# Kernel optimization log

Measured on AMD Instinct MI355X. Metric: run time of the kernel, lower is better.

## Reference

```python
import jax, jax.numpy as jnp
import numpy as np

B, T, HID = 1, 4096, 1024
H, HKV, D = 16, 4, 64          # query heads, kv heads, head_dim
G = H // HKV                    # gqa groups; repeat '(h g)' -> q head idx = h*G + g
EPS = 1e-6
SCALE = 1.0 / np.sqrt(D)


def setup_inputs() -> dict:
    key = jax.random.key(0)
    ks = jax.random.split(key, 8)
    hidden_states = jax.random.normal(ks[0], (B, T, HID), dtype=jnp.float32)
    # real rotary tables, shape [1, T, D//2]
    inv_freq = 1.0 / (10000.0 ** (jnp.arange(0, D // 2, dtype=jnp.float32) / (D // 2)))
    theta = jnp.arange(T, dtype=jnp.float32)[:, None] * inv_freq[None, :]
    cos = jnp.cos(theta)[None]
    sin = jnp.sin(theta)[None]
    s = 1.0 / np.sqrt(HID)
    Wq = jax.random.normal(ks[1], (HID, H * D), dtype=jnp.float32) * s
    Wk = jax.random.normal(ks[2], (HID, HKV * D), dtype=jnp.float32) * s
    Wv = jax.random.normal(ks[3], (HID, HKV * D), dtype=jnp.float32) * s
    Wo = jax.random.normal(ks[4], (H * D, HID), dtype=jnp.float32) * s
    q_norm_w = jnp.ones((D,), dtype=jnp.float32)
    k_norm_w = jnp.ones((D,), dtype=jnp.float32)
    return dict(hidden_states=hidden_states, cos=cos, sin=sin, Wq=Wq, Wk=Wk,
                Wv=Wv, Wo=Wo, q_norm_w=q_norm_w, k_norm_w=k_norm_w)


def _rmsnorm(x, w):
    xf = x.astype(jnp.float32)
    n = xf * jax.lax.rsqrt(jnp.mean(xf * xf, axis=-1, keepdims=True) + EPS)
    return (n * w).astype(x.dtype)


def _rope(x, cos, sin):
    # x: [b, t, h, d]; cos/sin: [1, t, d//2] -> [1, t, 1, d//2]
    half = x.shape[-1] // 2
    x1, x2 = x[..., :half], x[..., half:]
    c = cos[:, :x.shape[1], None, :]
    s = sin[:, :x.shape[1], None, :]
    return jnp.concatenate([x1 * c - x2 * s, x1 * s + x2 * c], axis=-1)


def reference(hidden_states, cos, sin, Wq, Wk, Wv, Wo, q_norm_w, k_norm_w):
    b, t, _ = hidden_states.shape
    q = (hidden_states @ Wq).reshape(b, t, H, D)
    k = (hidden_states @ Wk).reshape(b, t, HKV, D)
    v = (hidden_states @ Wv).reshape(b, t, HKV, D)
    q = _rmsnorm(q, q_norm_w)
    k = _rmsnorm(k, k_norm_w)
    q = _rope(q, cos, sin)
    k = _rope(k, cos, sin)
    # GQA without materializing repeated K/V: q head idx = kv_head*G + group
    qg = q.reshape(b, t, HKV, G, D)
    scores = jnp.einsum('bqhgd,bkhd->bhgqk', qg, k) * SCALE
    causal = jnp.tril(jnp.ones((t, t), dtype=bool))  # flex block_mask = causal decoder mask
    scores = jnp.where(causal, scores, jnp.finfo(scores.dtype).min)
    p = jax.nn.softmax(scores, axis=-1)
    out = jnp.einsum('bhgqk,bkhd->bqhgd', p, v).reshape(b, t, H * D)
    return out @ Wo
```

## Files before the change

kernel.cpp:

```cpp
#include <hip/hip_runtime.h>
#include <stdint.h>

#define TT 4096
#define HIDD 1024

typedef __attribute__((ext_vector_type(4))) float f32x4;
typedef __attribute__((ext_vector_type(8))) short s16x8;

static constexpr float kEps = 1e-6f;
static constexpr float kCsc = 0.125f * 1.44269504088896f;

static constexpr size_t OFF_HS   = 0;
static constexpr size_t OFF_WQKV = 8388608;
static constexpr size_t OFF_WO   = 11534336;
static constexpr size_t OFF_QKV  = 13631488;
static constexpr size_t OFF_Q    = 0;
static constexpr size_t OFF_K    = 8388608;
static constexpr size_t OFF_VT   = 38797312;
static constexpr size_t OFF_O    = 13631488;

__device__ __forceinline__ unsigned int pk_bf16(float a, float b) {
  union { float f; unsigned int u; } x, y;
  x.f = a; y.f = b;
  unsigned int lo = (x.u + 0x7fffu + ((x.u >> 16) & 1u)) >> 16;
  unsigned int hi = (y.u + 0x7fffu + ((y.u >> 16) & 1u)) >> 16;
  return (lo & 0xffffu) | (hi << 16);
}
__device__ __forceinline__ unsigned short bf16_1(float a) {
  union { float f; unsigned int u; } x; x.f = a;
  return (unsigned short)((x.u + 0x7fffu + ((x.u >> 16) & 1u)) >> 16);
}
__device__ __forceinline__ unsigned int cvtpk(float lo, float hi) {
  unsigned int r;
  asm("v_cvt_pk_bf16_f32 %0, %1, %2" : "=v"(r) : "v"(lo), "v"(hi));
  return r;
}
__device__ __forceinline__ void gload16(const void* g, void* l) {
  __builtin_amdgcn_global_load_lds(
      (const __attribute__((address_space(1))) unsigned int*)g,
      (__attribute__((address_space(3))) unsigned int*)l, 16, 0, 0);
}

__global__ void k_convert_hs(const float* __restrict__ hs, unsigned short* __restrict__ out) {
  int idx = blockIdx.x * 256 + threadIdx.x;
  int t = idx >> 7, kc = idx & 127;
  const float4* src = (const float4*)(hs + (size_t)t * HIDD + kc * 8);
  float4 a = src[0], b = src[1];
  int kcs = (kc & ~7) | ((kc & 7) ^ (t & 7));
  uint4 w;
  w.x = pk_bf16(a.x, a.y); w.y = pk_bf16(a.z, a.w);
  w.z = pk_bf16(b.x, b.y); w.w = pk_bf16(b.z, b.w);
  *(uint4*)(out + (size_t)t * HIDD + kcs * 8) = w;
}

__global__ void k_convert_w_all(const float* __restrict__ Wq, const float* __restrict__ Wk,
                                const float* __restrict__ Wv, const float* __restrict__ Wo,
                                unsigned short* __restrict__ wqkv, unsigned short* __restrict__ wo_t) {
  int b = blockIdx.x, tid = threadIdx.x;
  const float* W; unsigned short* outT; int nshift, idx;
  if (b < 512)      { W = Wq; outT = wqkv;                nshift = 10; idx = b * 256 + tid; }
  else if (b < 640) { W = Wk; outT = wqkv + 1024 * 1024;  nshift = 8;  idx = (b - 512) * 256 + tid; }
  else if (b < 768) { W = Wv; outT = wqkv + 1280 * 1024;  nshift = 8;  idx = (b - 640) * 256 + tid; }
  else              { W = Wo; outT = wo_t;                nshift = 10; idx = (b - 768) * 256 + tid; }
  int ncols = 1 << nshift;
  int kc = idx >> nshift, n = idx & (ncols - 1);
  float v[8];
#pragma unroll
  for (int e = 0; e < 8; ++e) v[e] = W[(size_t)(kc * 8 + e) * ncols + n];
  int kcs = (kc & ~7) | ((kc & 7) ^ (n & 7));
  uint4 w;
  w.x = pk_bf16(v[0], v[1]); w.y = pk_bf16(v[2], v[3]);
  w.z = pk_bf16(v[4], v[5]); w.w = pk_bf16(v[6], v[7]);
  *(uint4*)(outT + (size_t)n * HIDD + kcs * 8) = w;
}

__global__ __launch_bounds__(256) void k_gemm(const unsigned short* __restrict__ A,
                                              const unsigned short* __restrict__ Bt,
                                              float* __restrict__ C, int M, int N, int K) {
  __shared__ __attribute__((aligned(16))) unsigned short As[2][128 * 64];
  __shared__ __attribute__((aligned(16))) unsigned short Bs[2][64 * 64];
  const int tid = threadIdx.x;
  const int m0 = blockIdx.y * 128, n0 = blockIdx.x * 64;
  const int wid = tid >> 6, lane = tid & 63;
  const int g = lane >> 4, qi = lane & 15;
  const int wr = wid >> 1, wc = wid & 1;
  const int srow = lane >> 3, schk = lane & 7;
  f32x4 acc[4][2] = {};
  const int nkt = K >> 6;

  auto STAGE = [&](int b, int k0) {
#pragma unroll
    for (int j = 0; j < 4; ++j) {
      int ra = j * 32 + wid * 8 + srow;
      gload16(A + (size_t)(m0 + ra) * K + k0 + schk * 8,
              (char*)&As[b][0] + j * 4096 + (wid << 10));
    }
#pragma unroll
    for (int j = 0; j < 2; ++j) {
      int rb = j * 32 + wid * 8 + srow;
      gload16(Bt + (size_t)(n0 + rb) * K + k0 + schk * 8,
              (char*)&Bs[b][0] + j * 4096 + (wid << 10));
    }
  };

  STAGE(0, 0);
  __syncthreads();
  int cur = 0;
  for (int kt = 0; kt < nkt; ++kt) {
    if (kt + 1 < nkt) STAGE(cur ^ 1, (kt + 1) << 6);
#pragma unroll
    for (int kh = 0; kh < 2; ++kh) {
      s16x8 af[4], bq[2];
#pragma unroll
      for (int i = 0; i < 4; ++i) {
        int rA = wr * 64 + i * 16 + qi;
        af[i] = *(const s16x8*)((const char*)&As[cur][0] + rA * 128 + ((((kh << 2) | g) ^ (rA & 7)) << 4));
      }
#pragma unroll
      for (int jn = 0; jn < 2; ++jn) {
        int rB = wc * 32 + jn * 16 + qi;
        bq[jn] = *(const s16x8*)((const char*)&Bs[cur][0] + rB * 128 + ((((kh << 2) | g) ^ (rB & 7)) << 4));
      }
      __builtin_amdgcn_s_setprio(1);
#pragma unroll
      for (int i = 0; i < 4; ++i)
#pragma unroll
        for (int jn = 0; jn < 2; ++jn)
          acc[i][jn] = __builtin_amdgcn_mfma_f32_16x16x32_bf16(af[i], bq[jn], acc[i][jn], 0, 0, 0);
      __builtin_amdgcn_s_setprio(0);
    }
    __syncthreads();
    cur ^= 1;
  }
#pragma unroll
  for (int i = 0; i < 4; ++i)
#pragma unroll
    for (int jn = 0; jn < 2; ++jn) {
      int row = m0 + wr * 64 + i * 16 + g * 4;
      int col = n0 + wc * 32 + jn * 16 + qi;
#pragma unroll
      for (int r = 0; r < 4; ++r)
        C[(size_t)(row + r) * N + col] = acc[i][jn][r];
    }
}

__global__ void k_prep(const float* __restrict__ qkv, const float* __restrict__ cosb,
                       const float* __restrict__ sinb, const float* __restrict__ qw,
                       const float* __restrict__ kw, unsigned short* __restrict__ qo,
                       unsigned short* __restrict__ ko) {
  int rowid = blockIdx.x * 4 + (threadIdx.x >> 6);
  int lane = threadIdx.x & 63;
  int t = rowid / 20, slot = rowid % 20;
  float x = qkv[(size_t)t * 1536 + slot * 64 + lane];
  float ss = x * x;
#pragma unroll
  for (int off = 32; off; off >>= 1) ss += __shfl_xor(ss, off);
  float n = x * rsqrtf(ss * (1.0f / 64.0f) + kEps);
  n *= (slot < 16) ? qw[lane] : kw[lane];
  float c = cosb[t * 32 + (lane & 31)];
  float s = sinb[t * 32 + (lane & 31)];
  float other = __shfl_xor(n, 32);
  float r = (lane < 32) ? (n * c - other * s) : (other * s + n * c);
  if (slot < 16) {
    unsigned short b = bf16_1(r * kCsc);
    qo[((size_t)slot * TT + t) * 64 + lane] = b;
  } else {
    unsigned short b = bf16_1(r);
    int hv = slot - 16;
    int d = (((lane >> 3) ^ (t & 7)) << 3) | (lane & 7);
    ko[((size_t)hv * TT + t) * 64 + d] = b;
  }
}

__global__ void k_vT(const float* __restrict__ qkv, unsigned short* __restrict__ vt) {
  __shared__ float tile[64][65];
  int t0 = blockIdx.x * 64, hv = blockIdx.y, tid = threadIdx.x;
  int cc = tid & 63, rr0 = tid >> 6;
#pragma unroll
  for (int i = 0; i < 16; ++i) {
    int r = rr0 * 16 + i;
    tile[r][cc] = qkv[(size_t)(t0 + r) * 1536 + 1280 + hv * 64 + cc];
  }
  __syncthreads();
#pragma unroll
  for (int jj = 0; jj < 2; ++jj) {
    int idx = jj * 256 + tid;
    int d = idx >> 3, tc = idx & 7;
    uint4 w;
    w.x = pk_bf16(tile[tc * 8 + 0][d], tile[tc * 8 + 1][d]);
    w.y = pk_bf16(tile[tc * 8 + 2][d], tile[tc * 8 + 3][d]);
    w.z = pk_bf16(tile[tc * 8 + 4][d], tile[tc * 8 + 5][d]);
    w.w = pk_bf16(tile[tc * 8 + 6][d], tile[tc * 8 + 7][d]);
    int tcs = tc ^ (d & 7);
    *(uint4*)(vt + ((size_t)hv * 64 + d) * TT + t0 + tcs * 8) = w;
  }
}

__global__ __launch_bounds__(512) void k_attn(const unsigned short* __restrict__ q,
                                              const unsigned short* __restrict__ kk,
                                              const unsigned short* __restrict__ vt,
                                              unsigned short* __restrict__ o) {
  __shared__ __attribute__((aligned(16))) unsigned short Kl[2][64 * 64];
  __shared__ __attribute__((aligned(16))) unsigned short Vl[2][64 * 64];
  __shared__ __attribute__((aligned(16))) unsigned short Pl[8][1536];
  const int tid = threadIdx.x;
  const int bid = blockIdx.x;
  const int work = (bid & 7) * 64 + (bid >> 3);
  const int h = work >> 5;
  const int i0 = work & 31;
  const int hv = h >> 2;
  const int wid = tid >> 6, lane = tid & 63, g = lane >> 4, qi = lane & 15;
  const int qt = (wid < 4) ? i0 : (63 - i0);
  const int smax = 63 - i0;
  char* pb = (char*)&Pl[wid][0];

  auto STAGE = [&](int b, int s) {
    const int kv0 = s * 64;
    const int r = wid * 8 + (lane >> 3), c8 = (lane & 7) * 8;
    gload16(kk + ((size_t)hv * TT + kv0 + r) * 64 + c8, (char*)&Kl[b][0] + (wid << 10));
    gload16(vt + ((size_t)hv * 64 + r) * TT + kv0 + c8, (char*)&Vl[b][0] + (wid << 10));
  };

  const int qg = qt * 64 + (wid & 3) * 16 + qi;
  s16x8 qf[2];
#pragma unroll
  for (int kh = 0; kh < 2; ++kh)
    qf[kh] = *(const s16x8*)(q + ((size_t)h * TT + qg) * 64 + kh * 32 + g * 8);
  f32x4 acc[4] = {};
  float l0 = 0.0f, l1 = 0.0f;

  STAGE(0, 0);
  __syncthreads();
  int cur = 0;
  for (int s = 0; s <= smax; ++s) {
    if (s < smax) STAGE(cur ^ 1, s + 1);
    if (s <= qt) {
      const int kv0 = s * 64;
      f32x4 sacc[4] = {};
#pragma unroll
      for (int kh = 0; kh < 2; ++kh) {
        s16x8 kf[4];
#pragma unroll
        for (int cf = 0; cf < 4; ++cf) {
          int row = cf * 16 + qi;
          kf[cf] = *(const s16x8*)((const char*)&Kl[cur][0] + row * 128 + ((((kh << 2) | g) ^ (row & 7)) << 4));
        }
        __builtin_amdgcn_s_setprio(1);
#pragma unroll
        for (int cf = 0; cf < 4; ++cf)
          sacc[cf] = __builtin_amdgcn_mfma_f32_16x16x32_bf16(kf[cf], qf[kh], sacc[cf], 0, 0, 0);
        __builtin_amdgcn_s_setprio(0);
      }
      float pv[16];
      if (s == qt) {
#pragma unroll
        for (int cf = 0; cf < 4; ++cf)
#pragma unroll
          for (int r = 0; r < 4; ++r) {
            float v = sacc[cf][r];
            if ((kv0 + cf * 16 + g * 4 + r) > qg) v = -1e30f;
            pv[cf * 4 + r] = v;
          }
      } else {
#pragma unroll
        for (int cf = 0; cf < 4; ++cf)
#pragma unroll
          for (int r = 0; r < 4; ++r) pv[cf * 4 + r] = sacc[cf][r];
      }
#pragma unroll
      for (int i = 0; i < 8; ++i) {
        float e0 = exp2f(pv[2 * i]), e1 = exp2f(pv[2 * i + 1]);
        pv[2 * i] = e0; pv[2 * i + 1] = e1;
        l0 += e0; l1 += e1;
      }
#pragma unroll
      for (int cf = 0; cf < 4; ++cf) {
        int chunk = cf * 2 + (g >> 1);
        int base = qi * 128 + ((chunk ^ (qi & 7)) << 4) + ((g & 1) << 3);
        uint2 pw;
        pw.x = cvtpk(pv[cf * 4 + 0], pv[cf * 4 + 1]);
        pw.y = cvtpk(pv[cf * 4 + 2], pv[cf * 4 + 3]);
        *(uint2*)(pb + base) = pw;
      }
#pragma unroll
      for (int kh = 0; kh < 2; ++kh) {
        s16x8 pf = *(const s16x8*)(pb + qi * 128 + ((((kh << 2) | g) ^ (qi & 7)) << 4));
        s16x8 vf[4];
#pragma unroll
        for (int cf = 0; cf < 4; ++cf) {
          int row = cf * 16 + qi;
          vf[cf] = *(const s16x8*)((const char*)&Vl[cur][0] + row * 128 + ((((kh << 2) | g) ^ (row & 7)) << 4));
        }
        __builtin_amdgcn_s_setprio(1);
#pragma unroll
        for (int cf = 0; cf < 4; ++cf)
          acc[cf] = __builtin_amdgcn_mfma_f32_16x16x32_bf16(vf[cf], pf, acc[cf], 0, 0, 0);
        __builtin_amdgcn_s_setprio(0);
      }
    }
    __syncthreads();
    cur ^= 1;
  }
  float l_run = l0 + l1;
  l_run += __shfl_xor(l_run, 16);
  l_run += __shfl_xor(l_run, 32);
  float inv = 1.0f / l_run;
#pragma unroll
  for (int cf = 0; cf < 4; ++cf) {
    int col = h * 64 + cf * 16 + g * 4;
    int chunk = col >> 3;
    int chs = (chunk & ~7) | ((chunk & 7) ^ (qg & 7));
    char* ob = (char*)o + (size_t)qg * 2048 + (chs << 4) + ((g & 1) << 3);
    *(unsigned int*)ob = cvtpk(acc[cf][0] * inv, acc[cf][1] * inv);
    *(unsigned int*)(ob + 4) = cvtpk(acc[cf][2] * inv, acc[cf][3] * inv);
  }
}

extern "C" void kernel_launch(void* const* d_in, const int* in_sizes, int n_in,
                              void* d_out, int out_size, void* d_ws, size_t ws_size,
                              hipStream_t stream) {
  const float* hs   = (const float*)d_in[0];
  const float* cosb = (const float*)d_in[1];
  const float* sinb = (const float*)d_in[2];
  const float* Wq   = (const float*)d_in[3];
  const float* Wk   = (const float*)d_in[4];
  const float* Wv   = (const float*)d_in[5];
  const float* Wo   = (const float*)d_in[6];
  const float* qw   = (const float*)d_in[7];
  const float* kw   = (const float*)d_in[8];
  char* ws = (char*)d_ws;
  unsigned short* hs_swz = (unsigned short*)(ws + OFF_HS);
  unsigned short* wqkv   = (unsigned short*)(ws + OFF_WQKV);
  unsigned short* wo_t   = (unsigned short*)(ws + OFF_WO);
  float*          qkv    = (float*)(ws + OFF_QKV);
  unsigned short* qbf    = (unsigned short*)(ws + OFF_Q);
  unsigned short* kbf    = (unsigned short*)(ws + OFF_K);
  unsigned short* vtb    = (unsigned short*)(ws + OFF_VT);
  unsigned short* obf    = (unsigned short*)(ws + OFF_O);

  k_convert_hs<<<2048, 256, 0, stream>>>(hs, hs_swz);
  k_convert_w_all<<<1280, 256, 0, stream>>>(Wq, Wk, Wv, Wo, wqkv, wo_t);
  k_gemm<<<dim3(24, 32), 256, 0, stream>>>(hs_swz, wqkv, qkv, 4096, 1536, 1024);
  k_prep<<<20480, 256, 0, stream>>>(qkv, cosb, sinb, qw, kw, qbf, kbf);
  k_vT<<<dim3(64, 4), 256, 0, stream>>>(qkv, vtb);
  k_attn<<<512, 512, 0, stream>>>(qbf, kbf, vtb, obf);
  k_gemm<<<dim3(16, 32), 256, 0, stream>>>(obf, wo_t, (float*)d_out, 4096, 1024, 1024);
}
```

Baseline: 141.0 us.

## Rewrite attention with 32x32x16 MFMA, register-resident P, and new work mapping

```diff
diff --git a/kernel.cpp b/kernel.cpp
--- a/kernel.cpp
+++ b/kernel.cpp
@@ -5,6 +5,7 @@
 #define HIDD 1024
 
 typedef __attribute__((ext_vector_type(4))) float f32x4;
+typedef __attribute__((ext_vector_type(16))) float f32x16;
 typedef __attribute__((ext_vector_type(8))) short s16x8;
 
 static constexpr float kEps = 1e-6f;
@@ -196,123 +197,124 @@
   }
 }
 
-__global__ __launch_bounds__(512) void k_attn(const unsigned short* __restrict__ q,
-                                              const unsigned short* __restrict__ kk,
-                                              const unsigned short* __restrict__ vt,
-                                              unsigned short* __restrict__ o) {
-  __shared__ __attribute__((aligned(16))) unsigned short Kl[2][64 * 64];
-  __shared__ __attribute__((aligned(16))) unsigned short Vl[2][64 * 64];
-  __shared__ __attribute__((aligned(16))) unsigned short Pl[8][1536];
+__global__ __launch_bounds__(256, 2) void k_attn(const unsigned short* __restrict__ q,
+                                                 const unsigned short* __restrict__ kk,
+                                                 const unsigned short* __restrict__ vt,
+                                                 unsigned short* __restrict__ o) {
+  __shared__ __attribute__((aligned(16))) char smem[57344];
   const int tid = threadIdx.x;
+  const int wid = tid >> 6, lane = tid & 63;
+  const int ln31 = lane & 31, hi = lane >> 5;
   const int bid = blockIdx.x;
-  const int work = (bid & 7) * 64 + (bid >> 3);
-  const int h = work >> 5;
-  const int i0 = work & 31;
-  const int hv = h >> 2;
-  const int wid = tid >> 6, lane = tid & 63, g = lane >> 4, qi = lane & 15;
-  const int qt = (wid < 4) ? i0 : (63 - i0);
-  const int smax = 63 - i0;
-  char* pb = (char*)&Pl[wid][0];
-
-  auto STAGE = [&](int b, int s) {
-    const int kv0 = s * 64;
-    const int r = wid * 8 + (lane >> 3), c8 = (lane & 7) * 8;
-    gload16(kk + ((size_t)hv * TT + kv0 + r) * 64 + c8, (char*)&Kl[b][0] + (wid << 10));
-    gload16(vt + ((size_t)hv * 64 + r) * TT + kv0 + c8, (char*)&Vl[b][0] + (wid << 10));
+  const int xcd = bid & 7;
+  const int s = bid >> 3;
+  const int hsel = s >> 5;
+  const int t0_ = (s & 31) ^ hsel;
+  const int j = (t0_ & 1) ? (t0_ >> 1) : (31 - (t0_ >> 1));
+  const int head = xcd * 2 + hsel;
+  const int hv = head >> 2;
+  const int u = 4 * j + wid;
+  const int qbase = u * 32;
+  const int eu = (u >> 1) + 1;
+  const int E = 2 * j + 2;
+
+  auto STAGE = [&](int b, int st) {
+    const int kv0 = st * 64;
+#pragma unroll
+    for (int p = 0; p < 2; ++p) {
+      int c = tid + p * 256;
+      int row = c >> 3, ch = c & 7;
+      gload16(kk + ((size_t)hv * TT + kv0 + row) * 64 + ch * 8,
+              smem + b * 8192 + c * 16);
+      gload16(vt + ((size_t)hv * 64 + row) * TT + kv0 + ch * 8,
+              smem + 16384 + b * 8192 + c * 16);
+    }
   };
 
-  const int qg = qt * 64 + (wid & 3) * 16 + qi;
-  s16x8 qf[2];
-#pragma unroll
-  for (int kh = 0; kh < 2; ++kh)
-    qf[kh] = *(const s16x8*)(q + ((size_t)h * TT + qg) * 64 + kh * 32 + g * 8);
-  f32x4 acc[4] = {};
-  float l0 = 0.0f, l1 = 0.0f;
+  s16x8 qf[4];
+#pragma unroll
+  for (int ks = 0; ks < 4; ++ks)
+    qf[ks] = *(const s16x8*)(q + ((size_t)head * TT + qbase + ln31) * 64 + ks * 16 + hi * 8);
+
+  f32x16 oacc[2] = {};
+  float lp0 = 0.0f, lp1 = 0.0f;
 
   STAGE(0, 0);
   __syncthreads();
   int cur = 0;
-  for (int s = 0; s <= smax; ++s) {
-    if (s < smax) STAGE(cur ^ 1, s + 1);
-    if (s <= qt) {
-      const int kv0 = s * 64;
-      f32x4 sacc[4] = {};
-#pragma unroll
-      for (int kh = 0; kh < 2; ++kh) {
-        s16x8 kf[4];
-#pragma unroll
-        for (int cf = 0; cf < 4; ++cf) {
-          int row = cf * 16 + qi;
-          kf[cf] = *(const s16x8*)((const char*)&Kl[cur][0] + row * 128 + ((((kh << 2) | g) ^ (row & 7)) << 4));
+  for (int st = 0; st < E; ++st) {
+    if (st + 1 < E) STAGE(cur ^ 1, st + 1);
+    if (st < eu) {
+      const int kv0 = st * 64;
+      const char* Kb = smem + cur * 8192;
+      const char* Vb = smem + 16384 + cur * 8192;
+      f32x16 sacc[2] = {};
+#pragma unroll
+      for (int T = 0; T < 2; ++T) {
+#pragma unroll
+        for (int ks = 0; ks < 4; ++ks) {
+          int row = T * 32 + ln31;
+          s16x8 kf = *(const s16x8*)(Kb + row * 128 + (((2 * ks + hi) ^ (row & 7)) << 4));
+          sacc[T] = __builtin_amdgcn_mfma_f32_32x32x16_bf16(kf, qf[ks], sacc[T], 0, 0, 0);
         }
-        __builtin_amdgcn_s_setprio(1);
-#pragma unroll
-        for (int cf = 0; cf < 4; ++cf)
-          sacc[cf] = __builtin_amdgcn_mfma_f32_16x16x32_bf16(kf[cf], qf[kh], sacc[cf], 0, 0, 0);
-        __builtin_amdgcn_s_setprio(0);
-      }
-      float pv[16];
-      if (s == qt) {
-#pragma unroll
-        for (int cf = 0; cf < 4; ++cf)
-#pragma unroll
-          for (int r = 0; r < 4; ++r) {
-            float v = sacc[cf][r];
-            if ((kv0 + cf * 16 + g * 4 + r) > qg) v = -1e30f;
-            pv[cf * 4 + r] = v;
+      }
+      float pv[32];
+      const bool diag = (st == eu - 1);
+      const int qg = qbase + ln31;
+#pragma unroll
+      for (int T = 0; T < 2; ++T)
+#pragma unroll
+        for (int r = 0; r < 16; ++r) {
+          float v = sacc[T][r];
+          if (diag) {
+            int kvg = kv0 + T * 32 + (r & 3) + 8 * (r >> 2) + 4 * hi;
+            if (kvg > qg) v = -1e30f;
           }
-      } else {
-#pragma unroll
-        for (int cf = 0; cf < 4; ++cf)
-#pragma unroll
-          for (int r = 0; r < 4; ++r) pv[cf * 4 + r] = sacc[cf][r];
-      }
-#pragma unroll
-      for (int i = 0; i < 8; ++i) {
-        float e0 = exp2f(pv[2 * i]), e1 = exp2f(pv[2 * i + 1]);
-        pv[2 * i] = e0; pv[2 * i + 1] = e1;
-        l0 += e0; l1 += e1;
-      }
-#pragma unroll
-      for (int cf = 0; cf < 4; ++cf) {
-        int chunk = cf * 2 + (g >> 1);
-        int base = qi * 128 + ((chunk ^ (qi & 7)) << 4) + ((g & 1) << 3);
-        uint2 pw;
-        pw.x = cvtpk(pv[cf * 4 + 0], pv[cf * 4 + 1]);
-        pw.y = cvtpk(pv[cf * 4 + 2], pv[cf * 4 + 3]);
-        *(uint2*)(pb + base) = pw;
-      }
-#pragma unroll
-      for (int kh = 0; kh < 2; ++kh) {
-        s16x8 pf = *(const s16x8*)(pb + qi * 128 + ((((kh << 2) | g) ^ (qi & 7)) << 4));
-        s16x8 vf[4];
-#pragma unroll
-        for (int cf = 0; cf < 4; ++cf) {
-          int row = cf * 16 + qi;
-          vf[cf] = *(const s16x8*)((const char*)&Vl[cur][0] + row * 128 + ((((kh << 2) | g) ^ (row & 7)) << 4));
+          float e = exp2f(v);
+          pv[T * 16 + r] = e;
+          if (r & 1) lp1 += e; else lp0 += e;
         }
-        __builtin_amdgcn_s_setprio(1);
-#pragma unroll
-        for (int cf = 0; cf < 4; ++cf)
-          acc[cf] = __builtin_amdgcn_mfma_f32_16x16x32_bf16(vf[cf], pf, acc[cf], 0, 0, 0);
-        __builtin_amdgcn_s_setprio(0);
+      s16x8 pa[4];
+#pragma unroll
+      for (int ks = 0; ks < 4; ++ks) {
+        const float* pg = pv + ks * 8;
+        unsigned w0 = cvtpk(pg[0], pg[1]);
+        unsigned w1 = cvtpk(pg[2], pg[3]);
+        unsigned w2 = cvtpk(pg[4], pg[5]);
+        unsigned w3 = cvtpk(pg[6], pg[7]);
+        asm("v_permlane32_swap_b32 %0, %1" : "+v"(w0), "+v"(w2));
+        asm("v_permlane32_swap_b32 %0, %1" : "+v"(w1), "+v"(w3));
+        union { uint4 u4; s16x8 v8; } cc;
+        cc.u4.x = w0; cc.u4.y = w1; cc.u4.z = w2; cc.u4.w = w3;
+        pa[ks] = cc.v8;
+      }
+#pragma unroll
+      for (int D = 0; D < 2; ++D) {
+#pragma unroll
+        for (int ks = 0; ks < 4; ++ks) {
+          int row = D * 32 + ln31;
+          s16x8 vf = *(const s16x8*)(Vb + row * 128 + (((2 * ks + hi) ^ (row & 7)) << 4));
+          oacc[D] = __builtin_amdgcn_mfma_f32_32x32x16_bf16(pa[ks], vf, oacc[D], 0, 0, 0);
+        }
       }
     }
     __syncthreads();
     cur ^= 1;
   }
-  float l_run = l0 + l1;
-  l_run += __shfl_xor(l_run, 16);
-  l_run += __shfl_xor(l_run, 32);
-  float inv = 1.0f / l_run;
-#pragma unroll
-  for (int cf = 0; cf < 4; ++cf) {
-    int col = h * 64 + cf * 16 + g * 4;
-    int chunk = col >> 3;
-    int chs = (chunk & ~7) | ((chunk & 7) ^ (qg & 7));
-    char* ob = (char*)o + (size_t)qg * 2048 + (chs << 4) + ((g & 1) << 3);
-    *(unsigned int*)ob = cvtpk(acc[cf][0] * inv, acc[cf][1] * inv);
-    *(unsigned int*)(ob + 4) = cvtpk(acc[cf][2] * inv, acc[cf][3] * inv);
+  float lfull = lp0 + lp1;
+  lfull += __shfl_xor(lfull, 32);
+  float invl = 1.0f / lfull;
+#pragma unroll
+  for (int r = 0; r < 16; ++r) {
+    int qoff = (r & 3) + 8 * (r >> 2) + 4 * hi;
+    float il = __shfl(invl, qoff);
+    int q_g = qbase + qoff;
+    size_t rowb = (size_t)q_g * 2048 + head * 128 + (lane & 7) * 2;
+#pragma unroll
+    for (int D = 0; D < 2; ++D) {
+      int ch = ((4 * D + (ln31 >> 3)) ^ (q_g & 7)) << 4;
+      *(unsigned short*)((char*)o + rowb + ch) = bf16_1(oacc[D][r] * il);
+    }
   }
 }
 
@@ -343,6 +345,6 @@
   k_gemm<<<dim3(24, 32), 256, 0, stream>>>(hs_swz, wqkv, qkv, 4096, 1536, 1024);
   k_prep<<<20480, 256, 0, stream>>>(qkv, cosb, sinb, qw, kw, qbf, kbf);
   k_vT<<<dim3(64, 4), 256, 0, stream>>>(qkv, vtb);
-  k_attn<<<512, 512, 0, stream>>>(qbf, kbf, vtb, obf);
+  k_attn<<<512, 256, 0, stream>>>(qbf, kbf, vtb, obf);
   k_gemm<<<dim3(16, 32), 256, 0, stream>>>(obf, wo_t, (float*)d_out, 4096, 1024, 1024);
 }
```

Result: slower. 169.8 us (+20.5%).

## Fuse QK RMSnorm+RoPE and V transpose into QKV GEMM epilogue

Applied to the files above, without the earlier changes.

```diff
diff --git a/kernel.cpp b/kernel.cpp
--- a/kernel.cpp
+++ b/kernel.cpp
@@ -13,11 +13,10 @@
 static constexpr size_t OFF_HS   = 0;
 static constexpr size_t OFF_WQKV = 8388608;
 static constexpr size_t OFF_WO   = 11534336;
-static constexpr size_t OFF_QKV  = 13631488;
-static constexpr size_t OFF_Q    = 0;
-static constexpr size_t OFF_K    = 8388608;
+static constexpr size_t OFF_Q    = 13631488;
+static constexpr size_t OFF_K    = 22020096;
+static constexpr size_t OFF_O    = 24117248;
 static constexpr size_t OFF_VT   = 38797312;
-static constexpr size_t OFF_O    = 13631488;
 
 __device__ __forceinline__ unsigned int pk_bf16(float a, float b) {
   union { float f; unsigned int u; } x, y;
@@ -25,10 +24,6 @@
   unsigned int lo = (x.u + 0x7fffu + ((x.u >> 16) & 1u)) >> 16;
   unsigned int hi = (y.u + 0x7fffu + ((y.u >> 16) & 1u)) >> 16;
   return (lo & 0xffffu) | (hi << 16);
-}
-__device__ __forceinline__ unsigned short bf16_1(float a) {
-  union { float f; unsigned int u; } x; x.f = a;
-  return (unsigned short)((x.u + 0x7fffu + ((x.u >> 16) & 1u)) >> 16);
 }
 __device__ __forceinline__ unsigned int cvtpk(float lo, float hi) {
   unsigned int r;
@@ -72,6 +67,148 @@
   w.x = pk_bf16(v[0], v[1]); w.y = pk_bf16(v[2], v[3]);
   w.z = pk_bf16(v[4], v[5]); w.w = pk_bf16(v[6], v[7]);
   *(uint4*)(outT + (size_t)n * HIDD + kcs * 8) = w;
+}
+
+__global__ __launch_bounds__(256) void k_gemm_qkv(const unsigned short* __restrict__ A,
+                                                  const unsigned short* __restrict__ Bt,
+                                                  const float* __restrict__ cosb,
+                                                  const float* __restrict__ sinb,
+                                                  const float* __restrict__ qw,
+                                                  const float* __restrict__ kw,
+                                                  unsigned short* __restrict__ qo,
+                                                  unsigned short* __restrict__ ko,
+                                                  unsigned short* __restrict__ vt) {
+  __shared__ __attribute__((aligned(16))) char smem[49152];
+  const int K = HIDD;
+  const int tid = threadIdx.x;
+  const int m0 = blockIdx.y * 128, slot = blockIdx.x, n0 = slot * 64;
+  const int wid = tid >> 6, lane = tid & 63;
+  const int g = lane >> 4, qi = lane & 15;
+  const int wr = wid >> 1, wc = wid & 1;
+  const int srow = lane >> 3, schk = lane & 7;
+  f32x4 acc[4][2] = {};
+  const int nkt = K >> 6;
+
+  auto STAGE = [&](int b, int k0) {
+#pragma unroll
+    for (int j = 0; j < 4; ++j) {
+      int ra = j * 32 + wid * 8 + srow;
+      gload16(A + (size_t)(m0 + ra) * K + k0 + schk * 8,
+              smem + b * 16384 + j * 4096 + (wid << 10));
+    }
+#pragma unroll
+    for (int j = 0; j < 2; ++j) {
+      int rb = j * 32 + wid * 8 + srow;
+      gload16(Bt + (size_t)(n0 + rb) * K + k0 + schk * 8,
+              smem + 32768 + b * 8192 + j * 4096 + (wid << 10));
+    }
+  };
+
+  STAGE(0, 0);
+  __syncthreads();
+  int cur = 0;
+  for (int kt = 0; kt < nkt; ++kt) {
+    if (kt + 1 < nkt) STAGE(cur ^ 1, (kt + 1) << 6);
+#pragma unroll
+    for (int kh = 0; kh < 2; ++kh) {
+      s16x8 af[4], bq[2];
+#pragma unroll
+      for (int i = 0; i < 4; ++i) {
+        int rA = wr * 64 + i * 16 + qi;
+        af[i] = *(const s16x8*)(smem + cur * 16384 + rA * 128 + ((((kh << 2) | g) ^ (rA & 7)) << 4));
+      }
+#pragma unroll
+      for (int jn = 0; jn < 2; ++jn) {
+        int rB = wc * 32 + jn * 16 + qi;
+        bq[jn] = *(const s16x8*)(smem + 32768 + cur * 8192 + rB * 128 + ((((kh << 2) | g) ^ (rB & 7)) << 4));
+      }
+      __builtin_amdgcn_s_setprio(1);
+#pragma unroll
+      for (int i = 0; i < 4; ++i)
+#pragma unroll
+        for (int jn = 0; jn < 2; ++jn)
+          acc[i][jn] = __builtin_amdgcn_mfma_f32_16x16x32_bf16(af[i], bq[jn], acc[i][jn], 0, 0, 0);
+      __builtin_amdgcn_s_setprio(0);
+    }
+    __syncthreads();
+    cur ^= 1;
+  }
+
+  float* Cs = (float*)smem;
+#pragma unroll
+  for (int i = 0; i < 4; ++i)
+#pragma unroll
+    for (int jn = 0; jn < 2; ++jn) {
+      int row = wr * 64 + i * 16 + g * 4;
+      int col = wc * 32 + jn * 16 + qi;
+#pragma unroll
+      for (int r = 0; r < 4; ++r)
+        Cs[(row + r) * 66 + col] = acc[i][jn][r];
+    }
+  __syncthreads();
+
+  if (slot < 20) {
+    const int lr = tid >> 1, hf = tid & 1;
+    const int t = m0 + lr;
+    const float* self_p = Cs + lr * 66 + hf * 32;
+    const float* oth_p  = Cs + lr * 66 + (1 - hf) * 32;
+    float ss = 0.0f;
+#pragma unroll
+    for (int e = 0; e < 32; ++e) { float v = self_p[e]; ss += v * v; }
+    ss += __shfl_xor(ss, 1);
+    const float rms = rsqrtf(ss * (1.0f / 64.0f) + kEps);
+    const float* wvec = (slot < 16) ? qw : kw;
+    const float outscale = (slot < 16) ? kCsc : 1.0f;
+    unsigned int u[16];
+#pragma unroll
+    for (int ee = 0; ee < 16; ++ee) {
+      float o2[2];
+#pragma unroll
+      for (int p = 0; p < 2; ++p) {
+        int e = 2 * ee + p;
+        float c = cosb[t * 32 + e];
+        float s = sinb[t * 32 + e];
+        float self = self_p[e] * rms * wvec[hf * 32 + e];
+        float oth  = oth_p[e]  * rms * wvec[(1 - hf) * 32 + e];
+        float r = hf ? (oth * s + self * c) : (self * c - oth * s);
+        o2[p] = r * outscale;
+      }
+      u[ee] = cvtpk(o2[0], o2[1]);
+    }
+    if (slot < 16) {
+      unsigned short* base = qo + ((size_t)slot * TT + t) * 64 + hf * 32;
+#pragma unroll
+      for (int cidx = 0; cidx < 4; ++cidx) {
+        uint4 w; w.x = u[cidx * 4]; w.y = u[cidx * 4 + 1]; w.z = u[cidx * 4 + 2]; w.w = u[cidx * 4 + 3];
+        *(uint4*)(base + cidx * 8) = w;
+      }
+    } else {
+      const int hv = slot - 16;
+      unsigned short* base = ko + ((size_t)hv * TT + t) * 64;
+#pragma unroll
+      for (int cidx = 0; cidx < 4; ++cidx) {
+        int gc = hf * 4 + cidx;
+        uint4 w; w.x = u[cidx * 4]; w.y = u[cidx * 4 + 1]; w.z = u[cidx * 4 + 2]; w.w = u[cidx * 4 + 3];
+        *(uint4*)(base + (gc ^ (t & 7)) * 8) = w;
+      }
+    }
+  } else {
+    const int hv = slot - 20;
+#pragma unroll
+    for (int tt = 0; tt < 2; ++tt)
+#pragma unroll
+      for (int jj = 0; jj < 2; ++jj) {
+        int idx = jj * 256 + tid;
+        int d = idx >> 3, tc = idx & 7;
+        uint4 w;
+        w.x = cvtpk(Cs[(tt * 64 + tc * 8 + 0) * 66 + d], Cs[(tt * 64 + tc * 8 + 1) * 66 + d]);
+        w.y = cvtpk(Cs[(tt * 64 + tc * 8 + 2) * 66 + d], Cs[(tt * 64 + tc * 8 + 3) * 66 + d]);
+        w.z = cvtpk(Cs[(tt * 64 + tc * 8 + 4) * 66 + d], Cs[(tt * 64 + tc * 8 + 5) * 66 + d]);
+        w.w = cvtpk(Cs[(tt * 64 + tc * 8 + 6) * 66 + d], Cs[(tt * 64 + tc * 8 + 7) * 66 + d]);
+        int tcs = tc ^ (d & 7);
+        *(uint4*)(vt + ((size_t)hv * 64 + d) * TT + m0 + tt * 64 + tcs * 8) = w;
+      }
+  }
 }
 
 __global__ __launch_bounds__(256) void k_gemm(const unsigned short* __restrict__ A,
@@ -142,58 +279,6 @@
       for (int r = 0; r < 4; ++r)
         C[(size_t)(row + r) * N + col] = acc[i][jn][r];
     }
-}
-
-__global__ void k_prep(const float* __restrict__ qkv, const float* __restrict__ cosb,
-                       const float* __restrict__ sinb, const float* __restrict__ qw,
-                       const float* __restrict__ kw, unsigned short* __restrict__ qo,
-                       unsigned short* __restrict__ ko) {
-  int rowid = blockIdx.x * 4 + (threadIdx.x >> 6);
-  int lane = threadIdx.x & 63;
-  int t = rowid / 20, slot = rowid % 20;
-  float x = qkv[(size_t)t * 1536 + slot * 64 + lane];
-  float ss = x * x;
-#pragma unroll
-  for (int off = 32; off; off >>= 1) ss += __shfl_xor(ss, off);
-  float n = x * rsqrtf(ss * (1.0f / 64.0f) + kEps);
-  n *= (slot < 16) ? qw[lane] : kw[lane];
-  float c = cosb[t * 32 + (lane & 31)];
-  float s = sinb[t * 32 + (lane & 31)];
-  float other = __shfl_xor(n, 32);
-  float r = (lane < 32) ? (n * c - other * s) : (other * s + n * c);
-  if (slot < 16) {
-    unsigned short b = bf16_1(r * kCsc);
-    qo[((size_t)slot * TT + t) * 64 + lane] = b;
-  } else {
-    unsigned short b = bf16_1(r);
-    int hv = slot - 16;
-    int d = (((lane >> 3) ^ (t & 7)) << 3) | (lane & 7);
-    ko[((size_t)hv * TT + t) * 64 + d] = b;
-  }
-}
-
-__global__ void k_vT(const float* __restrict__ qkv, unsigned short* __restrict__ vt) {
-  __shared__ float tile[64][65];
-  int t0 = blockIdx.x * 64, hv = blockIdx.y, tid = threadIdx.x;
-  int cc = tid & 63, rr0 = tid >> 6;
-#pragma unroll
-  for (int i = 0; i < 16; ++i) {
-    int r = rr0 * 16 + i;
-    tile[r][cc] = qkv[(size_t)(t0 + r) * 1536 + 1280 + hv * 64 + cc];
-  }
-  __syncthreads();
-#pragma unroll
-  for (int jj = 0; jj < 2; ++jj) {
-    int idx = jj * 256 + tid;
-    int d = idx >> 3, tc = idx & 7;
-    uint4 w;
-    w.x = pk_bf16(tile[tc * 8 + 0][d], tile[tc * 8 + 1][d]);
-    w.y = pk_bf16(tile[tc * 8 + 2][d], tile[tc * 8 + 3][d]);
-    w.z = pk_bf16(tile[tc * 8 + 4][d], tile[tc * 8 + 5][d]);
-    w.w = pk_bf16(tile[tc * 8 + 6][d], tile[tc * 8 + 7][d]);
-    int tcs = tc ^ (d & 7);
-    *(uint4*)(vt + ((size_t)hv * 64 + d) * TT + t0 + tcs * 8) = w;
-  }
 }
 
 __global__ __launch_bounds__(512) void k_attn(const unsigned short* __restrict__ q,
@@ -332,7 +417,6 @@
   unsigned short* hs_swz = (unsigned short*)(ws + OFF_HS);
   unsigned short* wqkv   = (unsigned short*)(ws + OFF_WQKV);
   unsigned short* wo_t   = (unsigned short*)(ws + OFF_WO);
-  float*          qkv    = (float*)(ws + OFF_QKV);
   unsigned short* qbf    = (unsigned short*)(ws + OFF_Q);
   unsigned short* kbf    = (unsigned short*)(ws + OFF_K);
   unsigned short* vtb    = (unsigned short*)(ws + OFF_VT);
@@ -340,9 +424,7 @@
 
   k_convert_hs<<<2048, 256, 0, stream>>>(hs, hs_swz);
   k_convert_w_all<<<1280, 256, 0, stream>>>(Wq, Wk, Wv, Wo, wqkv, wo_t);
-  k_gemm<<<dim3(24, 32), 256, 0, stream>>>(hs_swz, wqkv, qkv, 4096, 1536, 1024);
-  k_prep<<<20480, 256, 0, stream>>>(qkv, cosb, sinb, qw, kw, qbf, kbf);
-  k_vT<<<dim3(64, 4), 256, 0, stream>>>(qkv, vtb);
+  k_gemm_qkv<<<dim3(24, 32), 256, 0, stream>>>(hs_swz, wqkv, cosb, sinb, qw, kw, qbf, kbf, vtb);
   k_attn<<<512, 512, 0, stream>>>(qbf, kbf, vtb, obf);
   k_gemm<<<dim3(16, 32), 256, 0, stream>>>(obf, wo_t, (float*)d_out, 4096, 1024, 1024);
 }
```

Result: faster. 131.1 us (median of 2 runs) (-7.0%).
